# Kernel tuning notes

Hardware: AMD Instinct MI355X
Metric: run time of the kernel (lower is better)

## Reference

```python
import jax, jax.numpy as jnp
import numpy as np

HEADS = 24
HEAD_DIM = 128
IP_SCALE = 1.0


def _rmsnorm(x, eps, weight=None):
    v = jnp.mean(x * x, axis=-1, keepdims=True)
    y = x * jax.lax.rsqrt(v + eps)
    return y * weight if weight is not None else y


def _rotate_half_interleaved(x):
    # diffusers apply_rotary_emb: pairs (x0, x1) -> (-x1, x0), interleaved
    x2 = x.reshape(*x.shape[:-1], -1, 2)
    rot = jnp.stack([-x2[..., 1], x2[..., 0]], axis=-1)
    return rot.reshape(x.shape)


def _sdpa(q, k, v):
    # q: [B,Sq,H,D], k/v: [B,Sk,H,D]
    scale = 1.0 / jnp.sqrt(jnp.asarray(HEAD_DIM, q.dtype))
    scores = jnp.einsum('bqhd,bkhd->bhqk', q, k) * scale
    p = jax.nn.softmax(scores, axis=-1)
    return jnp.einsum('bhqk,bkhd->bqhd', p, v)


def setup_inputs() -> dict:
    key = jax.random.key(0)
    ks = jax.random.split(key, 10)
    B, S, HID, CAD, T = 1, 2048, 3072, 4096, 128
    sc = 0.02
    return {
        'hidden_states': jax.random.normal(ks[0], (B, S, HID), jnp.float32),
        'cos': jnp.cos(jax.random.normal(ks[1], (S, HEAD_DIM), jnp.float32)),
        'sin': jnp.sin(jax.random.normal(ks[1], (S, HEAD_DIM), jnp.float32)),
        'ip_hidden': jax.random.normal(ks[2], (B, T, CAD), jnp.float32),
        'Wq': jax.random.normal(ks[3], (HID, HID), jnp.float32) * sc,
        'bq': jnp.zeros((HID,), jnp.float32),
        'Wk': jax.random.normal(ks[4], (HID, HID), jnp.float32) * sc,
        'bk': jnp.zeros((HID,), jnp.float32),
        'Wv': jax.random.normal(ks[5], (HID, HID), jnp.float32) * sc,
        'bv': jnp.zeros((HID,), jnp.float32),
        'norm_q_w': jnp.ones((HEAD_DIM,), jnp.float32),
        'norm_k_w': jnp.ones((HEAD_DIM,), jnp.float32),
        'Wk_ip': jax.random.normal(ks[6], (HID, CAD), jnp.float32) * sc,
        'Wv_ip': jax.random.normal(ks[7], (HID, CAD), jnp.float32) * sc,
    }


def reference(hidden_states, cos, sin, ip_hidden, Wq, bq, Wk, bk, Wv, bv,
              norm_q_w, norm_k_w, Wk_ip, Wv_ip):
    B, S, HID = hidden_states.shape
    # QKV projections (FLUX attn has bias=True)
    q = (hidden_states @ Wq.T + bq).reshape(B, S, HEADS, HEAD_DIM)
    k = (hidden_states @ Wk.T + bk).reshape(B, S, HEADS, HEAD_DIM)
    v = (hidden_states @ Wv.T + bv).reshape(B, S, HEADS, HEAD_DIM)
    # QK RMSNorm (affine, eps=1e-6 in FLUX)
    q = _rmsnorm(q, 1e-6, norm_q_w)
    k = _rmsnorm(k, 1e-6, norm_k_w)
    # RoPE (sequence_dim=1): cos/sin [S, D] -> broadcast over batch/heads
    c = cos[None, :, None, :]
    s = sin[None, :, None, :]
    q = q * c + _rotate_half_interleaved(q) * s
    k = k * c + _rotate_half_interleaved(k) * s
    out = _sdpa(q, k, v).reshape(B, S, HID)
    # IP-adapter branch
    T = ip_hidden.shape[1]
    ip_k = (ip_hidden @ Wk_ip.T).reshape(B, T, HEADS, HEAD_DIM)
    ip_v = (ip_hidden @ Wv_ip.T).reshape(B, T, HEADS, HEAD_DIM)
    ip_k = _rmsnorm(ip_k, 1e-5)
    ip_v = _rmsnorm(ip_v, 1e-5)
    ip_attn = _sdpa(q, ip_k, ip_v).reshape(B, S, HID)
    return out + IP_SCALE * ip_attn
```

## Files before the change

kernel.cpp:

```cpp
#include <hip/hip_runtime.h>
#include <stdint.h>

typedef unsigned short u16;
typedef __bf16 bf16x8 __attribute__((ext_vector_type(8)));
typedef float f32x4 __attribute__((ext_vector_type(4)));

#define HEADS 24
#define HD 128
#define S_LEN 2048
#define HID 3072

__device__ __forceinline__ u16 f2bf(float f) {
  union { float f; uint32_t u; } a; a.f = f;
  return (u16)((a.u + 0x7FFFu + ((a.u >> 16) & 1u)) >> 16);
}

__device__ __forceinline__ void gload16(const u16* g, u16* lds) {
  __builtin_amdgcn_global_load_lds(
      (const __attribute__((address_space(1))) void*)g,
      (__attribute__((address_space(3))) void*)lds, 16, 0, 0);
}

__global__ __launch_bounds__(256) void k_f2bf(const float* __restrict__ in,
                                              u16* __restrict__ out, int n4) {
  int i = blockIdx.x * 256 + threadIdx.x;
  if (i >= n4) return;
  float4 v = ((const float4*)in)[i];
  uint2 pk;
  pk.x = (uint32_t)f2bf(v.x) | ((uint32_t)f2bf(v.y) << 16);
  pk.y = (uint32_t)f2bf(v.z) | ((uint32_t)f2bf(v.w) << 16);
  ((uint2*)out)[i] = pk;
}

__global__ __launch_bounds__(256) void k_gemm_bt(
    const u16* __restrict__ A,
    const u16* __restrict__ B0, const u16* __restrict__ B1, const u16* __restrict__ B2,
    const float* __restrict__ bias0, const float* __restrict__ bias1, const float* __restrict__ bias2,
    float* __restrict__ C0, float* __restrict__ C1, float* __restrict__ C2,
    int N, int K, int atomic_split)
{
  const int z = blockIdx.z;
  const u16* __restrict__ B = (z == 0) ? B0 : (z == 1 ? B1 : B2);
  const float* __restrict__ bias = (z == 0) ? bias0 : (z == 1 ? bias1 : bias2);
  float* __restrict__ C = (z == 0) ? C0 : (z == 1 ? C1 : C2);
  const int m0 = atomic_split ? 0 : blockIdx.x * 128;
  const int n0 = blockIdx.y * 128;
  const int kb = atomic_split ? blockIdx.x * atomic_split : 0;
  const int ke = atomic_split ? kb + atomic_split : K;
  const int tid = threadIdx.x, l = tid & 63, w = tid >> 6;
  const int wm = w >> 1, wn = w & 1;
  const int lr = l & 15, lg = l >> 4;

  __shared__ u16 Al[128 * 32];
  __shared__ u16 Bl[128 * 32];

  f32x4 acc[4][4];
#pragma unroll
  for (int m = 0; m < 4; m++)
#pragma unroll
    for (int n = 0; n < 4; n++) acc[m][n] = f32x4{0.f, 0.f, 0.f, 0.f};

  const int srow = l >> 2, scol = (l & 3) * 8;
  const u16* Ab = A + (size_t)(m0 + srow) * K + scol;
  const u16* Bb = B + (size_t)(n0 + srow) * K + scol;
  const u16* af = &Al[(wm * 64 + lr) * 32 + lg * 8];
  const u16* bf = &Bl[(wn * 64 + lr) * 32 + lg * 8];

  for (int k0 = kb; k0 < ke; k0 += 32) {
    if (k0 != kb) __syncthreads();
#pragma unroll
    for (int j = 0; j < 2; j++) {
      const int c = j * 4 + w;
      gload16(Ab + (size_t)c * 16 * K + k0, &Al[c * 512]);
      gload16(Bb + (size_t)c * 16 * K + k0, &Bl[c * 512]);
    }
    __syncthreads();
    bf16x8 a[4], b[4];
#pragma unroll
    for (int m = 0; m < 4; m++) a[m] = *(const bf16x8*)(af + m * 16 * 32);
#pragma unroll
    for (int n = 0; n < 4; n++) b[n] = *(const bf16x8*)(bf + n * 16 * 32);
#pragma unroll
    for (int m = 0; m < 4; m++)
#pragma unroll
      for (int n = 0; n < 4; n++)
        acc[m][n] = __builtin_amdgcn_mfma_f32_16x16x32_bf16(a[m], b[n], acc[m][n], 0, 0, 0);
  }

  if (atomic_split) {
#pragma unroll
    for (int m = 0; m < 4; m++) {
      const int row = m0 + wm * 64 + m * 16 + lg * 4;
#pragma unroll
      for (int n = 0; n < 4; n++) {
        const int col = n0 + wn * 64 + n * 16 + lr;
#pragma unroll
        for (int r = 0; r < 4; r++)
          atomicAdd(&C[(size_t)(row + r) * N + col], acc[m][n][r]);
      }
    }
  } else {
#pragma unroll
    for (int m = 0; m < 4; m++) {
      const int row = m0 + wm * 64 + m * 16 + lg * 4;
#pragma unroll
      for (int n = 0; n < 4; n++) {
        const int col = n0 + wn * 64 + n * 16 + lr;
        const float bs = bias[col];
#pragma unroll
        for (int r = 0; r < 4; r++)
          C[(size_t)(row + r) * N + col] = acc[m][n][r] + bs;
      }
    }
  }
}

__global__ __launch_bounds__(256) void k_norm_rope(
    const float* __restrict__ Qraw, const float* __restrict__ Kraw,
    const float* __restrict__ cosp, const float* __restrict__ sinp,
    const float* __restrict__ wq, const float* __restrict__ wk,
    u16* __restrict__ Qh, u16* __restrict__ Kh)
{
  const int isK = blockIdx.y;
  const float* __restrict__ src = isK ? Kraw : Qraw;
  const float* __restrict__ wgt = isK ? wk : wq;
  u16* __restrict__ dst = isK ? Kh : Qh;
  const float scl = isK ? 1.0f : 0.08838834764831845f;
  const int w4 = threadIdx.x >> 6, l = threadIdx.x & 63;
  const int row = blockIdx.x * 4 + w4;
  const int s = row / 24, h = row - s * 24;
  const float2 x = *(const float2*)&src[(size_t)s * HID + h * HD + 2 * l];
  float ss = x.x * x.x + x.y * x.y;
#pragma unroll
  for (int off = 32; off; off >>= 1) ss += __shfl_xor(ss, off);
  const float rn = rsqrtf(ss * (1.0f / 128.0f) + 1e-6f);
  const float w0 = wgt[2 * l], w1 = wgt[2 * l + 1];
  const float c0 = cosp[s * HD + 2 * l], c1 = cosp[s * HD + 2 * l + 1];
  const float s0 = sinp[s * HD + 2 * l], s1 = sinp[s * HD + 2 * l + 1];
  const float y0 = x.x * rn * w0, y1 = x.y * rn * w1;
  const float o0 = (y0 * c0 - y1 * s0) * scl;
  const float o1 = (y1 * c1 + y0 * s1) * scl;
  const uint32_t pk = (uint32_t)f2bf(o0) | ((uint32_t)f2bf(o1) << 16);
  *(uint32_t*)&dst[((size_t)h * S_LEN + s) * HD + 2 * l] = pk;
}

__global__ __launch_bounds__(256) void k_ip_norm(
    const float* __restrict__ Kraw, const float* __restrict__ Vraw,
    u16* __restrict__ Kh, float* __restrict__ Vn)
{
  const int isV = blockIdx.y;
  const float* __restrict__ src = isV ? Vraw : Kraw;
  const int w4 = threadIdx.x >> 6, l = threadIdx.x & 63;
  const int row = blockIdx.x * 4 + w4;
  const int t = row / 24, h = row - t * 24;
  const float2 x = *(const float2*)&src[(size_t)t * HID + h * HD + 2 * l];
  float ss = x.x * x.x + x.y * x.y;
#pragma unroll
  for (int off = 32; off; off >>= 1) ss += __shfl_xor(ss, off);
  const float rn = rsqrtf(ss * (1.0f / 128.0f) + 1e-5f);
  const float o0 = x.x * rn, o1 = x.y * rn;
  if (isV) {
    *(float2*)&Vn[(size_t)t * HID + h * HD + 2 * l] = make_float2(o0, o1);
  } else {
    const uint32_t pk = (uint32_t)f2bf(o0) | ((uint32_t)f2bf(o1) << 16);
    *(uint32_t*)&Kh[((size_t)h * 128 + t) * HD + 2 * l] = pk;
  }
}

__global__ __launch_bounds__(256) void k_transpose(
    const float* __restrict__ X, u16* __restrict__ Y, int S)
{
  const int h = blockIdx.z, d0 = blockIdx.y * 32, s0 = blockIdx.x * 32;
  __shared__ float tile[32][33];
  const int c = threadIdx.x & 31, rb = threadIdx.x >> 5;
#pragma unroll
  for (int i = 0; i < 4; i++) {
    const int r = rb + i * 8;
    tile[r][c] = X[(size_t)(s0 + r) * HID + h * HD + d0 + c];
  }
  __syncthreads();
#pragma unroll
  for (int i = 0; i < 4; i++) {
    const int r = rb + i * 8;
    Y[((size_t)h * HD + d0 + r) * S + s0 + c] = f2bf(tile[c][r]);
  }
}

__global__ __launch_bounds__(256) void k_attn(
    const u16* __restrict__ Q, const u16* __restrict__ K, const u16* __restrict__ Vt,
    float* __restrict__ Out, int kv_len, int add)
{
  const int h = blockIdx.y;
  const int q0 = blockIdx.x * 64;
  const int tid = threadIdx.x, w = tid >> 6, l = tid & 63;
  const int lr = l & 15, lg = l >> 4;

  __shared__ u16 Kl[64][136];
  __shared__ u16 Vl[128][88];
  __shared__ u16 Pl[4][16][88];

  bf16x8 qf[4];
  {
    const u16* qp = &Q[((size_t)h * S_LEN + q0 + w * 16 + lr) * HD];
#pragma unroll
    for (int db = 0; db < 4; db++) qf[db] = *(const bf16x8*)&qp[db * 32 + lg * 8];
  }

  float m_[4], ls[4];
  f32x4 acc[8];
#pragma unroll
  for (int r = 0; r < 4; r++) { m_[r] = -1e30f; ls[r] = 0.f; }
#pragma unroll
  for (int nb = 0; nb < 8; nb++) acc[nb] = f32x4{0.f, 0.f, 0.f, 0.f};

  for (int kv0 = 0; kv0 < kv_len; kv0 += 64) {
#pragma unroll
    for (int i = 0; i < 4; i++) {
      const int c = tid + i * 256;
      { const int r = c >> 4, o = (c & 15) * 8;
        *(uint4*)&Kl[r][o] = *(const uint4*)&K[((size_t)h * kv_len + kv0 + r) * HD + o]; }
      { const int r = c >> 3, o = (c & 7) * 8;
        *(uint4*)&Vl[r][o] = *(const uint4*)&Vt[((size_t)h * HD + r) * kv_len + kv0 + o]; }
    }
    __syncthreads();

    f32x4 sf[4];
#pragma unroll
    for (int kb = 0; kb < 4; kb++) {
      f32x4 s = f32x4{0.f, 0.f, 0.f, 0.f};
#pragma unroll
      for (int db = 0; db < 4; db++) {
        bf16x8 b = *(const bf16x8*)&Kl[kb * 16 + lr][db * 32 + lg * 8];
        s = __builtin_amdgcn_mfma_f32_16x16x32_bf16(qf[db], b, s, 0, 0, 0);
      }
      sf[kb] = s;
    }

    float pv[4][4], rescv[4];
#pragma unroll
    for (int r = 0; r < 4; r++) {
      float tm = fmaxf(fmaxf(sf[0][r], sf[1][r]), fmaxf(sf[2][r], sf[3][r]));
#pragma unroll
      for (int off = 8; off; off >>= 1) tm = fmaxf(tm, __shfl_xor(tm, off));
      const float mn = fmaxf(m_[r], tm);
      const float resc = __expf(m_[r] - mn);
      float ps = 0.f;
#pragma unroll
      for (int kb = 0; kb < 4; kb++) { const float p = __expf(sf[kb][r] - mn); pv[kb][r] = p; ps += p; }
#pragma unroll
      for (int off = 8; off; off >>= 1) ps += __shfl_xor(ps, off);
      ls[r] = ls[r] * resc + ps;
      m_[r] = mn; rescv[r] = resc;
    }
#pragma unroll
    for (int nb = 0; nb < 8; nb++)
#pragma unroll
      for (int r = 0; r < 4; r++) acc[nb][r] *= rescv[r];

#pragma unroll
    for (int kb = 0; kb < 4; kb++)
#pragma unroll
      for (int r = 0; r < 4; r++)
        Pl[w][lg * 4 + r][kb * 16 + lr] = f2bf(pv[kb][r]);


#pragma unroll
    for (int kb = 0; kb < 2; kb++) {
      bf16x8 a = *(const bf16x8*)&Pl[w][lr][kb * 32 + lg * 8];
#pragma unroll
      for (int nb = 0; nb < 8; nb++) {
        bf16x8 b = *(const bf16x8*)&Vl[nb * 16 + lr][kb * 32 + lg * 8];
        acc[nb] = __builtin_amdgcn_mfma_f32_16x16x32_bf16(a, b, acc[nb], 0, 0, 0);
      }
    }
    __syncthreads();
  }

  float inv[4];
#pragma unroll
  for (int r = 0; r < 4; r++) inv[r] = 1.0f / ls[r];
#pragma unroll
  for (int nb = 0; nb < 8; nb++)
#pragma unroll
    for (int r = 0; r < 4; r++) {
      const int row = q0 + w * 16 + lg * 4 + r;
      const int col = h * HD + nb * 16 + lr;
      const size_t idx = (size_t)row * HID + col;
      const float v = acc[nb][r] * inv[r];
      if (add) Out[idx] += v; else Out[idx] = v;
    }
}

extern "C" void kernel_launch(void* const* d_in, const int* in_sizes, int n_in,
                              void* d_out, int out_size, void* d_ws, size_t ws_size,
                              hipStream_t stream) {
  const float* hs   = (const float*)d_in[0];
  const float* cosp = (const float*)d_in[1];
  const float* sinp = (const float*)d_in[2];
  const float* iph  = (const float*)d_in[3];
  const float* Wq   = (const float*)d_in[4];
  const float* bq   = (const float*)d_in[5];
  const float* Wk   = (const float*)d_in[6];
  const float* bk   = (const float*)d_in[7];
  const float* Wv   = (const float*)d_in[8];
  const float* bv   = (const float*)d_in[9];
  const float* nqw  = (const float*)d_in[10];
  const float* nkw  = (const float*)d_in[11];
  const float* Wkip = (const float*)d_in[12];
  const float* Wvip = (const float*)d_in[13];
  float* out = (float*)d_out;

  uint8_t* base = (uint8_t*)d_ws;
  size_t off = 0;
  auto alloc = [&](size_t bytes) { uint8_t* p = base + off; off += (bytes + 255) & ~(size_t)255; return p; };

  u16* X16 = (u16*)alloc(2048ull * 3072 * 2);
  uint8_t* regionB = base + off;
  u16* W16q  = (u16*)alloc(3072ull * 3072 * 2);
  u16* W16k  = (u16*)alloc(3072ull * 3072 * 2);
  u16* W16v  = (u16*)alloc(3072ull * 3072 * 2);
  u16* Wip16k = (u16*)alloc(3072ull * 4096 * 2);
  u16* Wip16v = (u16*)alloc(3072ull * 4096 * 2);
  u16* ip16   = (u16*)alloc(128ull * 4096 * 2);
  float* Qraw = (float*)alloc(2048ull * 3072 * 4);
  float* Kraw = (float*)alloc(2048ull * 3072 * 4);
  float* Vraw = (float*)alloc(2048ull * 3072 * 4);
  float* ipKraw = (float*)alloc(128ull * 3072 * 4);
  float* ipVraw = (float*)alloc(128ull * 3072 * 4);

  uint8_t* dp = regionB;
  auto allocD = [&](size_t bytes) { uint8_t* p = dp; dp += (bytes + 255) & ~(size_t)255; return p; };
  u16* Qh   = (u16*)allocD(24ull * 2048 * 128 * 2);
  u16* Kh   = (u16*)allocD(24ull * 2048 * 128 * 2);
  u16* Vt   = (u16*)allocD(24ull * 128 * 2048 * 2);
  u16* ipKh = (u16*)allocD(24ull * 128 * 128 * 2);
  u16* ipVt = (u16*)allocD(24ull * 128 * 128 * 2);
  float* ipVn = (float*)allocD(128ull * 3072 * 4);

  k_f2bf<<<6144, 256, 0, stream>>>(hs, X16, 1572864);
  k_f2bf<<<9216, 256, 0, stream>>>(Wq, W16q, 2359296);
  k_f2bf<<<9216, 256, 0, stream>>>(Wk, W16k, 2359296);
  k_f2bf<<<9216, 256, 0, stream>>>(Wv, W16v, 2359296);
  k_f2bf<<<12288, 256, 0, stream>>>(Wkip, Wip16k, 3145728);
  k_f2bf<<<12288, 256, 0, stream>>>(Wvip, Wip16v, 3145728);
  k_f2bf<<<512, 256, 0, stream>>>(iph, ip16, 131072);

  hipMemsetAsync(ipKraw, 0, 128ull * 3072 * 4, stream);
  hipMemsetAsync(ipVraw, 0, 128ull * 3072 * 4, stream);

  k_gemm_bt<<<dim3(16, 24, 3), 256, 0, stream>>>(X16, W16q, W16k, W16v, bq, bk, bv,
                                                 Qraw, Kraw, Vraw, 3072, 3072, 0);
  k_gemm_bt<<<dim3(4, 24, 2), 256, 0, stream>>>(ip16, Wip16k, Wip16v, Wip16v, bq, bq, bq,
                                                ipKraw, ipVraw, ipVraw, 3072, 4096, 1024);

  k_norm_rope<<<dim3(12288, 2), 256, 0, stream>>>(Qraw, Kraw, cosp, sinp, nqw, nkw, Qh, Kh);
  k_ip_norm<<<dim3(768, 2), 256, 0, stream>>>(ipKraw, ipVraw, ipKh, ipVn);
  k_transpose<<<dim3(64, 4, 24), 256, 0, stream>>>(Vraw, Vt, 2048);
  k_transpose<<<dim3(4, 4, 24), 256, 0, stream>>>(ipVn, ipVt, 128);

  k_attn<<<dim3(32, 24), 256, 0, stream>>>(Qh, Kh, Vt, out, 2048, 0);
  k_attn<<<dim3(32, 24), 256, 0, stream>>>(Qh, ipKh, ipVt, out, 128, 1);
}
```

Baseline: 687.2 us.

## Fuse conversion, norm, transpose and dual attention kernels; remap GEMM blocks across XCDs

```diff
diff --git a/kernel.cpp b/kernel.cpp
--- a/kernel.cpp
+++ b/kernel.cpp
@@ -21,15 +21,31 @@
       (__attribute__((address_space(3))) void*)lds, 16, 0, 0);
 }
 
-__global__ __launch_bounds__(256) void k_f2bf(const float* __restrict__ in,
-                                              u16* __restrict__ out, int n4) {
-  int i = blockIdx.x * 256 + threadIdx.x;
-  if (i >= n4) return;
-  float4 v = ((const float4*)in)[i];
-  uint2 pk;
-  pk.x = (uint32_t)f2bf(v.x) | ((uint32_t)f2bf(v.y) << 16);
-  pk.y = (uint32_t)f2bf(v.z) | ((uint32_t)f2bf(v.w) << 16);
-  ((uint2*)out)[i] = pk;
+struct ConvSeg { const float* in; void* out; int n4; int mode; };
+struct ConvArgs { ConvSeg s[9]; };
+
+__global__ __launch_bounds__(256) void k_convert_all(ConvArgs a) {
+  const int gid = blockIdx.x * 256 + threadIdx.x;
+  const int stride = gridDim.x * 256;
+#pragma unroll
+  for (int sg = 0; sg < 9; sg++) {
+    const int n = a.s[sg].n4;
+    if (a.s[sg].mode == 0) {
+      const float* __restrict__ in = a.s[sg].in;
+      u16* __restrict__ out = (u16*)a.s[sg].out;
+      for (int i = gid; i < n; i += stride) {
+        float4 v = ((const float4*)in)[i];
+        uint2 pk;
+        pk.x = (uint32_t)f2bf(v.x) | ((uint32_t)f2bf(v.y) << 16);
+        pk.y = (uint32_t)f2bf(v.z) | ((uint32_t)f2bf(v.w) << 16);
+        ((uint2*)out)[i] = pk;
+      }
+    } else {
+      float4* __restrict__ out = (float4*)a.s[sg].out;
+      const float4 z = make_float4(0.f, 0.f, 0.f, 0.f);
+      for (int i = gid; i < n; i += stride) out[i] = z;
+    }
+  }
 }
 
 __global__ __launch_bounds__(256) void k_gemm_bt(
@@ -39,13 +55,21 @@
     float* __restrict__ C0, float* __restrict__ C1, float* __restrict__ C2,
     int N, int K, int atomic_split)
 {
-  const int z = blockIdx.z;
+  const int orig = blockIdx.x + gridDim.x * (blockIdx.y + gridDim.y * blockIdx.z);
+  const int nwg = gridDim.x * gridDim.y * gridDim.z;
+  const int cpx = nwg >> 3;
+  const int wg = (orig & 7) * cpx + (orig >> 3);
+  const int bx = wg % gridDim.x;
+  const int rem = wg / gridDim.x;
+  const int by = rem % gridDim.y;
+  const int z = rem / gridDim.y;
+
   const u16* __restrict__ B = (z == 0) ? B0 : (z == 1 ? B1 : B2);
   const float* __restrict__ bias = (z == 0) ? bias0 : (z == 1 ? bias1 : bias2);
   float* __restrict__ C = (z == 0) ? C0 : (z == 1 ? C1 : C2);
-  const int m0 = atomic_split ? 0 : blockIdx.x * 128;
-  const int n0 = blockIdx.y * 128;
-  const int kb = atomic_split ? blockIdx.x * atomic_split : 0;
+  const int m0 = atomic_split ? 0 : bx * 128;
+  const int n0 = by * 128;
+  const int kb = atomic_split ? bx * atomic_split : 0;
   const int ke = atomic_split ? kb + atomic_split : K;
   const int tid = threadIdx.x, l = tid & 63, w = tid >> 6;
   const int wm = w >> 1, wn = w & 1;
@@ -115,62 +139,68 @@
   }
 }
 
-__global__ __launch_bounds__(256) void k_norm_rope(
+__global__ __launch_bounds__(256) void k_norms(
     const float* __restrict__ Qraw, const float* __restrict__ Kraw,
+    const float* __restrict__ ipKraw, const float* __restrict__ ipVraw,
     const float* __restrict__ cosp, const float* __restrict__ sinp,
     const float* __restrict__ wq, const float* __restrict__ wk,
-    u16* __restrict__ Qh, u16* __restrict__ Kh)
+    u16* __restrict__ Qh, u16* __restrict__ Kh,
+    u16* __restrict__ ipKh, float* __restrict__ ipVn)
 {
-  const int isK = blockIdx.y;
-  const float* __restrict__ src = isK ? Kraw : Qraw;
-  const float* __restrict__ wgt = isK ? wk : wq;
-  u16* __restrict__ dst = isK ? Kh : Qh;
-  const float scl = isK ? 1.0f : 0.08838834764831845f;
+  const int y = blockIdx.y;
   const int w4 = threadIdx.x >> 6, l = threadIdx.x & 63;
-  const int row = blockIdx.x * 4 + w4;
-  const int s = row / 24, h = row - s * 24;
-  const float2 x = *(const float2*)&src[(size_t)s * HID + h * HD + 2 * l];
-  float ss = x.x * x.x + x.y * x.y;
-#pragma unroll
-  for (int off = 32; off; off >>= 1) ss += __shfl_xor(ss, off);
-  const float rn = rsqrtf(ss * (1.0f / 128.0f) + 1e-6f);
-  const float w0 = wgt[2 * l], w1 = wgt[2 * l + 1];
-  const float c0 = cosp[s * HD + 2 * l], c1 = cosp[s * HD + 2 * l + 1];
-  const float s0 = sinp[s * HD + 2 * l], s1 = sinp[s * HD + 2 * l + 1];
-  const float y0 = x.x * rn * w0, y1 = x.y * rn * w1;
-  const float o0 = (y0 * c0 - y1 * s0) * scl;
-  const float o1 = (y1 * c1 + y0 * s1) * scl;
-  const uint32_t pk = (uint32_t)f2bf(o0) | ((uint32_t)f2bf(o1) << 16);
-  *(uint32_t*)&dst[((size_t)h * S_LEN + s) * HD + 2 * l] = pk;
-}
-
-__global__ __launch_bounds__(256) void k_ip_norm(
-    const float* __restrict__ Kraw, const float* __restrict__ Vraw,
-    u16* __restrict__ Kh, float* __restrict__ Vn)
+  if (y < 2) {
+    const int isK = y;
+    const float* __restrict__ src = isK ? Kraw : Qraw;
+    const float* __restrict__ wgt = isK ? wk : wq;
+    u16* __restrict__ dst = isK ? Kh : Qh;
+    const float scl = isK ? 1.0f : 0.08838834764831845f;
+    const int row = blockIdx.x * 4 + w4;
+    const int s = row / 24, h = row - s * 24;
+    const float2 x = *(const float2*)&src[(size_t)s * HID + h * HD + 2 * l];
+    float ss = x.x * x.x + x.y * x.y;
+#pragma unroll
+    for (int off = 32; off; off >>= 1) ss += __shfl_xor(ss, off);
+    const float rn = rsqrtf(ss * (1.0f / 128.0f) + 1e-6f);
+    const float w0 = wgt[2 * l], w1 = wgt[2 * l + 1];
+    const float c0 = cosp[s * HD + 2 * l], c1 = cosp[s * HD + 2 * l + 1];
+    const float s0 = sinp[s * HD + 2 * l], s1 = sinp[s * HD + 2 * l + 1];
+    const float y0 = x.x * rn * w0, y1 = x.y * rn * w1;
+    const float o0 = (y0 * c0 - y1 * s0) * scl;
+    const float o1 = (y1 * c1 + y0 * s1) * scl;
+    const uint32_t pk = (uint32_t)f2bf(o0) | ((uint32_t)f2bf(o1) << 16);
+    *(uint32_t*)&dst[((size_t)h * S_LEN + s) * HD + 2 * l] = pk;
+  } else {
+    if (blockIdx.x >= 768) return;
+    const int isV = (y == 3);
+    const float* __restrict__ src = isV ? ipVraw : ipKraw;
+    const int row = blockIdx.x * 4 + w4;
+    const int t = row / 24, h = row - t * 24;
+    const float2 x = *(const float2*)&src[(size_t)t * HID + h * HD + 2 * l];
+    float ss = x.x * x.x + x.y * x.y;
+#pragma unroll
+    for (int off = 32; off; off >>= 1) ss += __shfl_xor(ss, off);
+    const float rn = rsqrtf(ss * (1.0f / 128.0f) + 1e-5f);
+    const float o0 = x.x * rn, o1 = x.y * rn;
+    if (isV) {
+      *(float2*)&ipVn[(size_t)t * HID + h * HD + 2 * l] = make_float2(o0, o1);
+    } else {
+      const uint32_t pk = (uint32_t)f2bf(o0) | ((uint32_t)f2bf(o1) << 16);
+      *(uint32_t*)&ipKh[((size_t)h * 128 + t) * HD + 2 * l] = pk;
+    }
+  }
+}
+
+__global__ __launch_bounds__(256) void k_transpose2(
+    const float* __restrict__ Vraw, const float* __restrict__ ipVn,
+    u16* __restrict__ Vt, u16* __restrict__ ipVt)
 {
-  const int isV = blockIdx.y;
-  const float* __restrict__ src = isV ? Vraw : Kraw;
-  const int w4 = threadIdx.x >> 6, l = threadIdx.x & 63;
-  const int row = blockIdx.x * 4 + w4;
-  const int t = row / 24, h = row - t * 24;
-  const float2 x = *(const float2*)&src[(size_t)t * HID + h * HD + 2 * l];
-  float ss = x.x * x.x + x.y * x.y;
-#pragma unroll
-  for (int off = 32; off; off >>= 1) ss += __shfl_xor(ss, off);
-  const float rn = rsqrtf(ss * (1.0f / 128.0f) + 1e-5f);
-  const float o0 = x.x * rn, o1 = x.y * rn;
-  if (isV) {
-    *(float2*)&Vn[(size_t)t * HID + h * HD + 2 * l] = make_float2(o0, o1);
-  } else {
-    const uint32_t pk = (uint32_t)f2bf(o0) | ((uint32_t)f2bf(o1) << 16);
-    *(uint32_t*)&Kh[((size_t)h * 128 + t) * HD + 2 * l] = pk;
-  }
-}
-
-__global__ __launch_bounds__(256) void k_transpose(
-    const float* __restrict__ X, u16* __restrict__ Y, int S)
-{
-  const int h = blockIdx.z, d0 = blockIdx.y * 32, s0 = blockIdx.x * 32;
+  const int h = blockIdx.z, d0 = blockIdx.y * 32;
+  const float* __restrict__ X;
+  u16* __restrict__ Y;
+  int S, s0;
+  if (blockIdx.x < 64) { X = Vraw; Y = Vt; S = 2048; s0 = blockIdx.x * 32; }
+  else                 { X = ipVn; Y = ipVt; S = 128; s0 = (blockIdx.x - 64) * 32; }
   __shared__ float tile[32][33];
   const int c = threadIdx.x & 31, rb = threadIdx.x >> 5;
 #pragma unroll
@@ -186,9 +216,11 @@
   }
 }
 
-__global__ __launch_bounds__(256) void k_attn(
-    const u16* __restrict__ Q, const u16* __restrict__ K, const u16* __restrict__ Vt,
-    float* __restrict__ Out, int kv_len, int add)
+__global__ __launch_bounds__(256) void k_attn2(
+    const u16* __restrict__ Q,
+    const u16* __restrict__ K1, const u16* __restrict__ Vt1,
+    const u16* __restrict__ K2, const u16* __restrict__ Vt2,
+    float* __restrict__ Out)
 {
   const int h = blockIdx.y;
   const int q0 = blockIdx.x * 64;
@@ -206,88 +238,91 @@
     for (int db = 0; db < 4; db++) qf[db] = *(const bf16x8*)&qp[db * 32 + lg * 8];
   }
 
-  float m_[4], ls[4];
-  f32x4 acc[8];
-#pragma unroll
-  for (int r = 0; r < 4; r++) { m_[r] = -1e30f; ls[r] = 0.f; }
-#pragma unroll
-  for (int nb = 0; nb < 8; nb++) acc[nb] = f32x4{0.f, 0.f, 0.f, 0.f};
-
-  for (int kv0 = 0; kv0 < kv_len; kv0 += 64) {
-#pragma unroll
-    for (int i = 0; i < 4; i++) {
-      const int c = tid + i * 256;
-      { const int r = c >> 4, o = (c & 15) * 8;
-        *(uint4*)&Kl[r][o] = *(const uint4*)&K[((size_t)h * kv_len + kv0 + r) * HD + o]; }
-      { const int r = c >> 3, o = (c & 7) * 8;
-        *(uint4*)&Vl[r][o] = *(const uint4*)&Vt[((size_t)h * HD + r) * kv_len + kv0 + o]; }
-    }
-    __syncthreads();
-
-    f32x4 sf[4];
-#pragma unroll
-    for (int kb = 0; kb < 4; kb++) {
-      f32x4 s = f32x4{0.f, 0.f, 0.f, 0.f};
-#pragma unroll
-      for (int db = 0; db < 4; db++) {
-        bf16x8 b = *(const bf16x8*)&Kl[kb * 16 + lr][db * 32 + lg * 8];
-        s = __builtin_amdgcn_mfma_f32_16x16x32_bf16(qf[db], b, s, 0, 0, 0);
-      }
-      sf[kb] = s;
-    }
-
-    float pv[4][4], rescv[4];
-#pragma unroll
-    for (int r = 0; r < 4; r++) {
-      float tm = fmaxf(fmaxf(sf[0][r], sf[1][r]), fmaxf(sf[2][r], sf[3][r]));
-#pragma unroll
-      for (int off = 8; off; off >>= 1) tm = fmaxf(tm, __shfl_xor(tm, off));
-      const float mn = fmaxf(m_[r], tm);
-      const float resc = __expf(m_[r] - mn);
-      float ps = 0.f;
-#pragma unroll
-      for (int kb = 0; kb < 4; kb++) { const float p = __expf(sf[kb][r] - mn); pv[kb][r] = p; ps += p; }
-#pragma unroll
-      for (int off = 8; off; off >>= 1) ps += __shfl_xor(ps, off);
-      ls[r] = ls[r] * resc + ps;
-      m_[r] = mn; rescv[r] = resc;
-    }
-#pragma unroll
-    for (int nb = 0; nb < 8; nb++)
-#pragma unroll
-      for (int r = 0; r < 4; r++) acc[nb][r] *= rescv[r];
-
-#pragma unroll
-    for (int kb = 0; kb < 4; kb++)
-#pragma unroll
-      for (int r = 0; r < 4; r++)
-        Pl[w][lg * 4 + r][kb * 16 + lr] = f2bf(pv[kb][r]);
-
-
-#pragma unroll
-    for (int kb = 0; kb < 2; kb++) {
-      bf16x8 a = *(const bf16x8*)&Pl[w][lr][kb * 32 + lg * 8];
-#pragma unroll
-      for (int nb = 0; nb < 8; nb++) {
-        bf16x8 b = *(const bf16x8*)&Vl[nb * 16 + lr][kb * 32 + lg * 8];
-        acc[nb] = __builtin_amdgcn_mfma_f32_16x16x32_bf16(a, b, acc[nb], 0, 0, 0);
-      }
-    }
-    __syncthreads();
-  }
-
-  float inv[4];
-#pragma unroll
-  for (int r = 0; r < 4; r++) inv[r] = 1.0f / ls[r];
+  auto attn_pass = [&](const u16* __restrict__ K, const u16* __restrict__ Vt,
+                       int kv_len, float* m_, float* ls, f32x4* acc) {
+    for (int kv0 = 0; kv0 < kv_len; kv0 += 64) {
+#pragma unroll
+      for (int i = 0; i < 4; i++) {
+        const int c = tid + i * 256;
+        { const int r = c >> 4, o = (c & 15) * 8;
+          *(uint4*)&Kl[r][o] = *(const uint4*)&K[((size_t)h * kv_len + kv0 + r) * HD + o]; }
+        { const int r = c >> 3, o = (c & 7) * 8;
+          *(uint4*)&Vl[r][o] = *(const uint4*)&Vt[((size_t)h * HD + r) * kv_len + kv0 + o]; }
+      }
+      __syncthreads();
+
+      f32x4 sf[4];
+#pragma unroll
+      for (int kb = 0; kb < 4; kb++) {
+        f32x4 s = f32x4{0.f, 0.f, 0.f, 0.f};
+#pragma unroll
+        for (int db = 0; db < 4; db++) {
+          bf16x8 b = *(const bf16x8*)&Kl[kb * 16 + lr][db * 32 + lg * 8];
+          s = __builtin_amdgcn_mfma_f32_16x16x32_bf16(qf[db], b, s, 0, 0, 0);
+        }
+        sf[kb] = s;
+      }
+
+      float pv[4][4], rescv[4];
+#pragma unroll
+      for (int r = 0; r < 4; r++) {
+        float tm = fmaxf(fmaxf(sf[0][r], sf[1][r]), fmaxf(sf[2][r], sf[3][r]));
+#pragma unroll
+        for (int off = 8; off; off >>= 1) tm = fmaxf(tm, __shfl_xor(tm, off));
+        const float mn = fmaxf(m_[r], tm);
+        const float resc = __expf(m_[r] - mn);
+        float ps = 0.f;
+#pragma unroll
+        for (int kb = 0; kb < 4; kb++) { const float p = __expf(sf[kb][r] - mn); pv[kb][r] = p; ps += p; }
+#pragma unroll
+        for (int off = 8; off; off >>= 1) ps += __shfl_xor(ps, off);
+        ls[r] = ls[r] * resc + ps;
+        m_[r] = mn; rescv[r] = resc;
+      }
+#pragma unroll
+      for (int nb = 0; nb < 8; nb++)
+#pragma unroll
+        for (int r = 0; r < 4; r++) acc[nb][r] *= rescv[r];
+
+#pragma unroll
+      for (int kb = 0; kb < 4; kb++)
+#pragma unroll
+        for (int r = 0; r < 4; r++)
+          Pl[w][lg * 4 + r][kb * 16 + lr] = f2bf(pv[kb][r]);
+
+#pragma unroll
+      for (int kb = 0; kb < 2; kb++) {
+        bf16x8 a = *(const bf16x8*)&Pl[w][lr][kb * 32 + lg * 8];
+#pragma unroll
+        for (int nb = 0; nb < 8; nb++) {
+          bf16x8 b = *(const bf16x8*)&Vl[nb * 16 + lr][kb * 32 + lg * 8];
+          acc[nb] = __builtin_amdgcn_mfma_f32_16x16x32_bf16(a, b, acc[nb], 0, 0, 0);
+        }
+      }
+      __syncthreads();
+    }
+  };
+
+  float m1[4], ls1[4], m2[4], ls2[4];
+  f32x4 acc1[8], acc2[8];
+#pragma unroll
+  for (int r = 0; r < 4; r++) { m1[r] = -1e30f; ls1[r] = 0.f; m2[r] = -1e30f; ls2[r] = 0.f; }
+#pragma unroll
+  for (int nb = 0; nb < 8; nb++) { acc1[nb] = f32x4{0.f, 0.f, 0.f, 0.f}; acc2[nb] = f32x4{0.f, 0.f, 0.f, 0.f}; }
+
+  attn_pass(K1, Vt1, 2048, m1, ls1, acc1);
+  attn_pass(K2, Vt2, 128,  m2, ls2, acc2);
+
+  float i1[4], i2[4];
+#pragma unroll
+  for (int r = 0; r < 4; r++) { i1[r] = 1.0f / ls1[r]; i2[r] = 1.0f / ls2[r]; }
 #pragma unroll
   for (int nb = 0; nb < 8; nb++)
 #pragma unroll
     for (int r = 0; r < 4; r++) {
       const int row = q0 + w * 16 + lg * 4 + r;
       const int col = h * HD + nb * 16 + lr;
-      const size_t idx = (size_t)row * HID + col;
-      const float v = acc[nb][r] * inv[r];
-      if (add) Out[idx] += v; else Out[idx] = v;
+      Out[(size_t)row * HID + col] = acc1[nb][r] * i1[r] + acc2[nb][r] * i2[r];
     }
 }
 
@@ -337,27 +372,26 @@
   u16* ipVt = (u16*)allocD(24ull * 128 * 128 * 2);
   float* ipVn = (float*)allocD(128ull * 3072 * 4);
 
-  k_f2bf<<<6144, 256, 0, stream>>>(hs, X16, 1572864);
-  k_f2bf<<<9216, 256, 0, stream>>>(Wq, W16q, 2359296);
-  k_f2bf<<<9216, 256, 0, stream>>>(Wk, W16k, 2359296);
-  k_f2bf<<<9216, 256, 0, stream>>>(Wv, W16v, 2359296);
-  k_f2bf<<<12288, 256, 0, stream>>>(Wkip, Wip16k, 3145728);
-  k_f2bf<<<12288, 256, 0, stream>>>(Wvip, Wip16v, 3145728);
-  k_f2bf<<<512, 256, 0, stream>>>(iph, ip16, 131072);
-
-  hipMemsetAsync(ipKraw, 0, 128ull * 3072 * 4, stream);
-  hipMemsetAsync(ipVraw, 0, 128ull * 3072 * 4, stream);
+  ConvArgs ca;
+  ca.s[0] = { hs,   (void*)X16,     1572864, 0 };
+  ca.s[1] = { Wq,   (void*)W16q,    2359296, 0 };
+  ca.s[2] = { Wk,   (void*)W16k,    2359296, 0 };
+  ca.s[3] = { Wv,   (void*)W16v,    2359296, 0 };
+  ca.s[4] = { Wkip, (void*)Wip16k,  3145728, 0 };
+  ca.s[5] = { Wvip, (void*)Wip16v,  3145728, 0 };
+  ca.s[6] = { iph,  (void*)ip16,    131072,  0 };
+  ca.s[7] = { nullptr, (void*)ipKraw, 98304, 1 };
+  ca.s[8] = { nullptr, (void*)ipVraw, 98304, 1 };
+  k_convert_all<<<2048, 256, 0, stream>>>(ca);
 
   k_gemm_bt<<<dim3(16, 24, 3), 256, 0, stream>>>(X16, W16q, W16k, W16v, bq, bk, bv,
                                                  Qraw, Kraw, Vraw, 3072, 3072, 0);
   k_gemm_bt<<<dim3(4, 24, 2), 256, 0, stream>>>(ip16, Wip16k, Wip16v, Wip16v, bq, bq, bq,
                                                 ipKraw, ipVraw, ipVraw, 3072, 4096, 1024);
 
-  k_norm_rope<<<dim3(12288, 2), 256, 0, stream>>>(Qraw, Kraw, cosp, sinp, nqw, nkw, Qh, Kh);
-  k_ip_norm<<<dim3(768, 2), 256, 0, stream>>>(ipKraw, ipVraw, ipKh, ipVn);
-  k_transpose<<<dim3(64, 4, 24), 256, 0, stream>>>(Vraw, Vt, 2048);
-  k_transpose<<<dim3(4, 4, 24), 256, 0, stream>>>(ipVn, ipVt, 128);
-
-  k_attn<<<dim3(32, 24), 256, 0, stream>>>(Qh, Kh, Vt, out, 2048, 0);
-  k_attn<<<dim3(32, 24), 256, 0, stream>>>(Qh, ipKh, ipVt, out, 128, 1);
-}
+  k_norms<<<dim3(12288, 4), 256, 0, stream>>>(Qraw, Kraw, ipKraw, ipVraw,
+                                              cosp, sinp, nqw, nkw, Qh, Kh, ipKh, ipVn);
+  k_transpose2<<<dim3(68, 4, 24), 256, 0, stream>>>(Vraw, ipVn, Vt, ipVt);
+
+  k_attn2<<<dim3(32, 24), 256, 0, stream>>>(Qh, Kh, Vt, ipKh, ipVt, out);
+}
```

New measurement: 650.6 us. -5.3%, faster.
